# Performance work log

Hardware: AMD Instinct MI355X
Metric: run time of the kernel (lower is better)

## Reference

```python
import jax, jax.numpy as jnp
import numpy as np

EPS = 1e-12  # F.normalize default eps

def _l2norm(x, axis):
    n = jnp.maximum(jnp.linalg.norm(x, axis=axis, keepdims=True), EPS)
    return x / n

def setup_inputs() -> dict:
    key = jax.random.key(0)
    k1, k2 = jax.random.split(key)
    B, G, D, K = 256, 100, 768, 128
    h = jax.random.normal(k1, (B, G, D), dtype=jnp.float32)
    duplicate_pooling = jax.random.normal(k2, (G, D, K), dtype=jnp.float32)
    out_extrap = jnp.zeros((B, G, K), dtype=jnp.float32)
    return {"h": h, "duplicate_pooling": duplicate_pooling, "out_extrap": out_extrap}

def reference(h, duplicate_pooling, out_extrap):
    # normalize=True: L2-normalize each h[:, i, :] over feature dim (dim=1 of the
    # flattened [B, D] view == last axis), and each w_i = W[i] over dim=0 (the D axis).
    hn = _l2norm(h, axis=-1)                       # [B, G, D]
    wn = _l2norm(duplicate_pooling, axis=1)        # [G, D, K]
    # Fused grouped batched GEMM over all G groups at once.
    out = jnp.einsum('bgd,gdk->bgk', hn, wn)       # [B, G, K]
    return out
```

## Files before the change

kernel.cpp:

```cpp
#include <hip/hip_runtime.h>
#include <hip/hip_bf16.h>

#define Gn   100
#define Bn   256
#define Dn   768
#define Kn   128
#define LDP  40

typedef __attribute__((ext_vector_type(8))) short short8;
typedef __attribute__((ext_vector_type(4))) float f32x4;

__device__ inline unsigned short f2b(float f) {
  union { float f; unsigned u; } v; v.f = f;
  unsigned r = v.u + 0x7FFFu + ((v.u >> 16) & 1u);
  return (unsigned short)(r >> 16);
}

__global__ __launch_bounds__(256) void hnorm_kernel(const float* __restrict__ h,
                                                    float* __restrict__ hinv) {
  const int row  = blockIdx.x * 4 + (threadIdx.x >> 6);
  const int lane = threadIdx.x & 63;
  const float4* p = (const float4*)(h + (size_t)row * Dn);
  float ssq = 0.f;
#pragma unroll
  for (int j = 0; j < 3; ++j) {
    float4 v = p[j * 64 + lane];
    ssq += v.x*v.x + v.y*v.y + v.z*v.z + v.w*v.w;
  }
#pragma unroll
  for (int off = 32; off > 0; off >>= 1) ssq += __shfl_down(ssq, off);
  if (lane == 0) hinv[row] = 1.0f / fmaxf(sqrtf(ssq), 1e-12f);
}

__global__ __launch_bounds__(256) void wssq_kernel(const float* __restrict__ W,
                                                   float* __restrict__ wssq) {
  const int g  = blockIdx.x;
  const int s  = blockIdx.y;
  const int t  = threadIdx.x;
  const int k  = t & 127;
  const int dh = t >> 7;
  const float* p = W + (size_t)g * (Dn * Kn) + (size_t)(s * 192 + dh * 96) * Kn + k;
  float ssq = 0.f;
#pragma unroll 8
  for (int i = 0; i < 96; ++i) { float v = p[(size_t)i * Kn]; ssq += v * v; }
  atomicAdd(&wssq[g * Kn + k], ssq);
}

__global__ __launch_bounds__(256) void gemm_kernel(
    const float* __restrict__ h, const float* __restrict__ W,
    const float* __restrict__ hinv, const float* __restrict__ wssq,
    float* __restrict__ out) {
  const int g    = blockIdx.z;
  const int mt   = blockIdx.x;
  const int nt   = blockIdx.y;
  const int t    = threadIdx.x;
  const int lane = t & 63;
  const int wave = t >> 6;
  const int wm   = wave >> 1, wn = wave & 1;

  __shared__ short Alds[64 * LDP];
  __shared__ short Blds[64 * LDP];

  f32x4 acc00 = {0.f,0.f,0.f,0.f};
  f32x4 acc01 = acc00, acc10 = acc00, acc11 = acc00;

  const int ar = t >> 2;
  const int ac = (t & 3) * 8;
  const float* aptr = h + ((size_t)(mt * 64 + ar) * Gn + g) * Dn + ac;
  const int bk = t & 63;
  const int bd = (t >> 6) * 8;
  const float* bptr = W + (size_t)g * (Dn * Kn) + (size_t)bd * Kn + nt * 64 + bk;

  const int quad = lane >> 4;
  const int koff = quad * 8;
  const int l15  = lane & 15;
  const int m0   = wm * 32 + l15;
  const int n0   = wn * 32 + l15;

  for (int kc = 0; kc < 24; ++kc) {
    const int d0 = kc * 32;
    float4 a0 = *(const float4*)(aptr + d0);
    float4 a1 = *(const float4*)(aptr + d0 + 4);
    float bv[8];
#pragma unroll
    for (int i = 0; i < 8; ++i) bv[i] = bptr[(size_t)(d0 + i) * Kn];

    if (kc) __syncthreads();

    union { unsigned short us[8]; short8 v; } pa;
    pa.us[0]=f2b(a0.x); pa.us[1]=f2b(a0.y); pa.us[2]=f2b(a0.z); pa.us[3]=f2b(a0.w);
    pa.us[4]=f2b(a1.x); pa.us[5]=f2b(a1.y); pa.us[6]=f2b(a1.z); pa.us[7]=f2b(a1.w);
    *(short8*)&Alds[ar * LDP + ac] = pa.v;

    union { unsigned short us[8]; short8 v; } pb;
#pragma unroll
    for (int i = 0; i < 8; ++i) pb.us[i] = f2b(bv[i]);
    *(short8*)&Blds[bk * LDP + bd] = pb.v;

    __syncthreads();

    short8 af0 = *(const short8*)&Alds[m0 * LDP + koff];
    short8 af1 = *(const short8*)&Alds[(m0 + 16) * LDP + koff];
    short8 bf0 = *(const short8*)&Blds[n0 * LDP + koff];
    short8 bf1 = *(const short8*)&Blds[(n0 + 16) * LDP + koff];

    acc00 = __builtin_amdgcn_mfma_f32_16x16x32_bf16(af0, bf0, acc00, 0, 0, 0);
    acc01 = __builtin_amdgcn_mfma_f32_16x16x32_bf16(af0, bf1, acc01, 0, 0, 0);
    acc10 = __builtin_amdgcn_mfma_f32_16x16x32_bf16(af1, bf0, acc10, 0, 0, 0);
    acc11 = __builtin_amdgcn_mfma_f32_16x16x32_bf16(af1, bf1, acc11, 0, 0, 0);
  }

  const int gk0 = g * Kn + nt * 64;
  const float wi0 = 1.0f / fmaxf(sqrtf(wssq[gk0 + n0]), 1e-12f);
  const float wi1 = 1.0f / fmaxf(sqrtf(wssq[gk0 + n0 + 16]), 1e-12f);

#pragma unroll
  for (int mi = 0; mi < 2; ++mi) {
#pragma unroll
    for (int r = 0; r < 4; ++r) {
      const int row = mt * 64 + wm * 32 + mi * 16 + quad * 4 + r;
      const float hs = hinv[(size_t)row * Gn + g];
      const float v0 = (mi ? acc10[r] : acc00[r]) * hs * wi0;
      const float v1 = (mi ? acc11[r] : acc01[r]) * hs * wi1;
      const size_t ob = ((size_t)row * Gn + g) * Kn + nt * 64;
      out[ob + wn * 32 + l15]      = v0;
      out[ob + wn * 32 + l15 + 16] = v1;
    }
  }
}

extern "C" void kernel_launch(void* const* d_in, const int* in_sizes, int n_in,
                              void* d_out, int out_size, void* d_ws, size_t ws_size,
                              hipStream_t stream) {
  const float* h = (const float*)d_in[0];
  const float* W = (const float*)d_in[1];
  float* out = (float*)d_out;

  float* hinv = (float*)d_ws;
  float* wssq = hinv + (size_t)Bn * Gn;

  hipMemsetAsync((void*)wssq, 0, (size_t)Gn * Kn * sizeof(float), stream);
  hipLaunchKernelGGL(hnorm_kernel, dim3((Bn * Gn) / 4), dim3(256), 0, stream, h, hinv);
  hipLaunchKernelGGL(wssq_kernel, dim3(Gn, 4), dim3(256), 0, stream, W, wssq);
  hipLaunchKernelGGL(gemm_kernel, dim3(4, 2, Gn), dim3(256), 0, stream,
                     h, W, hinv, wssq, out);
}
```

Measured before the change: 205.9 us.

## Fuse norm computations into GEMM and double-buffer LDS with register prefetch

Drops the separate h-norm and W column-norm kernels and the memset. Each GEMM block now accumulates sums of squares from the fp32 values it already loads, reduces them through shared memory, and applies the inverse norms in the epilogue. This removes two extra full passes over h and W plus three launches. The k-loop also double-buffers LDS and prefetches the next chunk into registers, which drops one barrier per iteration and overlaps loads with MFMA, at the cost of more registers and twice the LDS.

```diff
diff --git a/kernel.cpp b/kernel.cpp
--- a/kernel.cpp
+++ b/kernel.cpp
@@ -1,5 +1,4 @@
 #include <hip/hip_runtime.h>
-#include <hip/hip_bf16.h>
 
 #define Gn   100
 #define Bn   256
@@ -16,39 +15,8 @@
   return (unsigned short)(r >> 16);
 }
 
-__global__ __launch_bounds__(256) void hnorm_kernel(const float* __restrict__ h,
-                                                    float* __restrict__ hinv) {
-  const int row  = blockIdx.x * 4 + (threadIdx.x >> 6);
-  const int lane = threadIdx.x & 63;
-  const float4* p = (const float4*)(h + (size_t)row * Dn);
-  float ssq = 0.f;
-#pragma unroll
-  for (int j = 0; j < 3; ++j) {
-    float4 v = p[j * 64 + lane];
-    ssq += v.x*v.x + v.y*v.y + v.z*v.z + v.w*v.w;
-  }
-#pragma unroll
-  for (int off = 32; off > 0; off >>= 1) ssq += __shfl_down(ssq, off);
-  if (lane == 0) hinv[row] = 1.0f / fmaxf(sqrtf(ssq), 1e-12f);
-}
-
-__global__ __launch_bounds__(256) void wssq_kernel(const float* __restrict__ W,
-                                                   float* __restrict__ wssq) {
-  const int g  = blockIdx.x;
-  const int s  = blockIdx.y;
-  const int t  = threadIdx.x;
-  const int k  = t & 127;
-  const int dh = t >> 7;
-  const float* p = W + (size_t)g * (Dn * Kn) + (size_t)(s * 192 + dh * 96) * Kn + k;
-  float ssq = 0.f;
-#pragma unroll 8
-  for (int i = 0; i < 96; ++i) { float v = p[(size_t)i * Kn]; ssq += v * v; }
-  atomicAdd(&wssq[g * Kn + k], ssq);
-}
-
-__global__ __launch_bounds__(256) void gemm_kernel(
+__global__ __launch_bounds__(256) void groupfc_kernel(
     const float* __restrict__ h, const float* __restrict__ W,
-    const float* __restrict__ hinv, const float* __restrict__ wssq,
     float* __restrict__ out) {
   const int g    = blockIdx.z;
   const int mt   = blockIdx.x;
@@ -58,8 +26,10 @@
   const int wave = t >> 6;
   const int wm   = wave >> 1, wn = wave & 1;
 
-  __shared__ short Alds[64 * LDP];
-  __shared__ short Blds[64 * LDP];
+  __shared__ short Alds[2][64 * LDP];
+  __shared__ short Blds[2][64 * LDP];
+  __shared__ float AssqL[64];
+  __shared__ float BssqL[4][64];
 
   f32x4 acc00 = {0.f,0.f,0.f,0.f};
   f32x4 acc01 = acc00, acc10 = acc00, acc11 = acc00;
@@ -77,51 +47,74 @@
   const int m0   = wm * 32 + l15;
   const int n0   = wn * 32 + l15;
 
+  float assq = 0.f, bssq = 0.f;
+
+  float4 a0 = *(const float4*)(aptr);
+  float4 a1 = *(const float4*)(aptr + 4);
+  float bv[8];
+#pragma unroll
+  for (int i = 0; i < 8; ++i) bv[i] = bptr[(size_t)i * Kn];
+
   for (int kc = 0; kc < 24; ++kc) {
-    const int d0 = kc * 32;
-    float4 a0 = *(const float4*)(aptr + d0);
-    float4 a1 = *(const float4*)(aptr + d0 + 4);
-    float bv[8];
+    float4 na0, na1;
+    float nbv[8];
+    if (kc < 23) {
+      const int d0 = (kc + 1) * 32;
+      na0 = *(const float4*)(aptr + d0);
+      na1 = *(const float4*)(aptr + d0 + 4);
 #pragma unroll
-    for (int i = 0; i < 8; ++i) bv[i] = bptr[(size_t)(d0 + i) * Kn];
+      for (int i = 0; i < 8; ++i) nbv[i] = bptr[(size_t)(d0 + i) * Kn];
+    }
 
-    if (kc) __syncthreads();
-
+    assq += a0.x*a0.x + a0.y*a0.y + a0.z*a0.z + a0.w*a0.w
+          + a1.x*a1.x + a1.y*a1.y + a1.z*a1.z + a1.w*a1.w;
     union { unsigned short us[8]; short8 v; } pa;
     pa.us[0]=f2b(a0.x); pa.us[1]=f2b(a0.y); pa.us[2]=f2b(a0.z); pa.us[3]=f2b(a0.w);
     pa.us[4]=f2b(a1.x); pa.us[5]=f2b(a1.y); pa.us[6]=f2b(a1.z); pa.us[7]=f2b(a1.w);
-    *(short8*)&Alds[ar * LDP + ac] = pa.v;
+    *(short8*)&Alds[kc & 1][ar * LDP + ac] = pa.v;
 
     union { unsigned short us[8]; short8 v; } pb;
 #pragma unroll
-    for (int i = 0; i < 8; ++i) pb.us[i] = f2b(bv[i]);
-    *(short8*)&Blds[bk * LDP + bd] = pb.v;
+    for (int i = 0; i < 8; ++i) { bssq += bv[i] * bv[i]; pb.us[i] = f2b(bv[i]); }
+    *(short8*)&Blds[kc & 1][bk * LDP + bd] = pb.v;
 
     __syncthreads();
 
-    short8 af0 = *(const short8*)&Alds[m0 * LDP + koff];
-    short8 af1 = *(const short8*)&Alds[(m0 + 16) * LDP + koff];
-    short8 bf0 = *(const short8*)&Blds[n0 * LDP + koff];
-    short8 bf1 = *(const short8*)&Blds[(n0 + 16) * LDP + koff];
+    short8 af0 = *(const short8*)&Alds[kc & 1][m0 * LDP + koff];
+    short8 af1 = *(const short8*)&Alds[kc & 1][(m0 + 16) * LDP + koff];
+    short8 bf0 = *(const short8*)&Blds[kc & 1][n0 * LDP + koff];
+    short8 bf1 = *(const short8*)&Blds[kc & 1][(n0 + 16) * LDP + koff];
 
     acc00 = __builtin_amdgcn_mfma_f32_16x16x32_bf16(af0, bf0, acc00, 0, 0, 0);
     acc01 = __builtin_amdgcn_mfma_f32_16x16x32_bf16(af0, bf1, acc01, 0, 0, 0);
     acc10 = __builtin_amdgcn_mfma_f32_16x16x32_bf16(af1, bf0, acc10, 0, 0, 0);
     acc11 = __builtin_amdgcn_mfma_f32_16x16x32_bf16(af1, bf1, acc11, 0, 0, 0);
+
+    a0 = na0; a1 = na1;
+#pragma unroll
+    for (int i = 0; i < 8; ++i) bv[i] = nbv[i];
   }
 
-  const int gk0 = g * Kn + nt * 64;
-  const float wi0 = 1.0f / fmaxf(sqrtf(wssq[gk0 + n0]), 1e-12f);
-  const float wi1 = 1.0f / fmaxf(sqrtf(wssq[gk0 + n0 + 16]), 1e-12f);
+  assq += __shfl_xor(assq, 1);
+  assq += __shfl_xor(assq, 2);
+  if ((t & 3) == 0) AssqL[ar] = assq;
+  BssqL[wave][bk] = bssq;
+  __syncthreads();
+
+  const float ws0 = BssqL[0][n0] + BssqL[1][n0] + BssqL[2][n0] + BssqL[3][n0];
+  const float ws1 = BssqL[0][n0+16] + BssqL[1][n0+16] + BssqL[2][n0+16] + BssqL[3][n0+16];
+  const float wi0 = 1.0f / fmaxf(sqrtf(ws0), 1e-12f);
+  const float wi1 = 1.0f / fmaxf(sqrtf(ws1), 1e-12f);
 
 #pragma unroll
   for (int mi = 0; mi < 2; ++mi) {
 #pragma unroll
     for (int r = 0; r < 4; ++r) {
-      const int row = mt * 64 + wm * 32 + mi * 16 + quad * 4 + r;
-      const float hs = hinv[(size_t)row * Gn + g];
+      const int lr  = wm * 32 + mi * 16 + quad * 4 + r;
+      const float hs = 1.0f / fmaxf(sqrtf(AssqL[lr]), 1e-12f);
       const float v0 = (mi ? acc10[r] : acc00[r]) * hs * wi0;
       const float v1 = (mi ? acc11[r] : acc01[r]) * hs * wi1;
+      const int row = mt * 64 + lr;
       const size_t ob = ((size_t)row * Gn + g) * Kn + nt * 64;
       out[ob + wn * 32 + l15]      = v0;
       out[ob + wn * 32 + l15 + 16] = v1;
@@ -135,13 +128,5 @@
   const float* h = (const float*)d_in[0];
   const float* W = (const float*)d_in[1];
   float* out = (float*)d_out;
-
-  float* hinv = (float*)d_ws;
-  float* wssq = hinv + (size_t)Bn * Gn;
-
-  hipMemsetAsync((void*)wssq, 0, (size_t)Gn * Kn * sizeof(float), stream);
-  hipLaunchKernelGGL(hnorm_kernel, dim3((Bn * Gn) / 4), dim3(256), 0, stream, h, hinv);
-  hipLaunchKernelGGL(wssq_kernel, dim3(Gn, 4), dim3(256), 0, stream, W, wssq);
-  hipLaunchKernelGGL(gemm_kernel, dim3(4, 2, Gn), dim3(256), 0, stream,
-                     h, W, hinv, wssq, out);
+  hipLaunchKernelGGL(groupfc_kernel, dim3(4, 2, Gn), dim3(256), 0, stream, h, W, out);
 }
```

Result: faster. 171.9 us (-16.5%).
